# Kernel tuning notes

Hardware: AMD Instinct MI355X
Metric: run time of the kernel (lower is better)

Reference implementation:

```python
import jax, jax.numpy as jnp
import numpy as np

B, CIN, COUT = 8, 8, 8
NX, NT = 512, 512
M1, M2 = 4, 4


def setup_inputs() -> dict:
    key = jax.random.key(0)
    k1, k2, k3 = jax.random.split(key, 3)
    scale = 1.0 / (CIN * COUT)
    x = jax.random.normal(k1, (B, CIN, NX, NT), dtype=jnp.float32)
    T = jnp.arange(NT, dtype=jnp.float32).reshape(1, NT)  # time grid
    X = jnp.arange(NX, dtype=jnp.float32).reshape(1, NX)  # space grid
    weights1_ri = scale * jax.random.uniform(k2, (CIN, COUT, M1, M2, 2), dtype=jnp.float32)
    weights2_ri = scale * jax.random.uniform(k3, (CIN, COUT, M1, M2, 2), dtype=jnp.float32)
    return {"x": x, "T": T, "X": X, "weights1_ri": weights1_ri, "weights2_ri": weights2_ri}


def reference(x, T, X, weights1_ri, weights2_ri):
    # subsample every other grid point (as in the torch forward)
    xs = x[:, :, ::2, ::2]                      # [B, Cin, Hs, Ws]
    tx = T[:, ::2]                              # [1, Ws]
    ty = X[:, ::2]                              # [1, Hs]
    dty = ty[0, 1] - ty[0, 0]
    dtx = tx[0, 1] - tx[0, 0]
    Hs, Ws = xs.shape[-2], xs.shape[-1]
    Wr = Ws // 2 + 1

    FW1 = jnp.fft.rfft2(xs)                     # [B, Cin, Hs, Wr] complex64

    two_pi_i = 2.0 * jnp.pi * 1j
    lam1 = (jnp.fft.fftfreq(Hs).astype(jnp.float32) / dty).astype(jnp.complex64) * two_pi_i   # [Hs]
    lam2 = (jnp.fft.rfftfreq(Ws).astype(jnp.float32) / dtx).astype(jnp.complex64) * two_pi_i  # [Wr]

    w1 = (weights1_ri[..., 0] + 1j * weights1_ri[..., 1]).astype(jnp.complex64)
    w2 = (weights2_ri[..., 0] + 1j * weights2_ri[..., 1]).astype(jnp.complex64)

    out2 = jnp.zeros((xs.shape[0], w1.shape[1], Hs, Wr), dtype=jnp.complex64)
    out2 = out2.at[:, :, :M1, :M2].set(
        jnp.einsum('bixy,ioxy->boxy', FW1[:, :, :M1, :M2], w1))
    out2 = out2.at[:, :, -M1:, :M2].set(
        jnp.einsum('bixy,ioxy->boxy', FW1[:, :, -M1:, :M2], w2))

    # inverse transform onto the FULL (non-subsampled) grid via complex exponentials.
    # Same math as the original rank-4 term6 einsum, factorized separably.
    E1 = jnp.exp(lam1[:, None] * X.astype(jnp.complex64).reshape(1, -1))  # [Hs, NX]
    E2 = jnp.exp(lam2[:, None] * T.astype(jnp.complex64).reshape(1, -1))  # [Wr, NT]

    tmp = jnp.einsum('boxw,xz->bozw', out2, E1)   # [B, Cout, NX, Wr]
    x2 = jnp.einsum('bozw,wi->bozi', tmp, E2)     # [B, Cout, NX, NT]
    return jnp.real(x2) / (Ws * Hs)
```

## Files before the change

### kernel.cpp

```cpp
#include <hip/hip_runtime.h>
#include <hip/hip_bf16.h>


#define PI2 6.283185307179586f

__device__ __forceinline__ float foldred(float u, float v, int msk, int lane) {
    float send = (lane & msk) ? u : v;
    float recv = __shfl_xor(send, msk, 64);
    return ((lane & msk) ? v : u) + recv;
}

__global__ void k_dft_t(const float* __restrict__ x, float* __restrict__ pf) {
    int gid  = blockIdx.x * blockDim.x + threadIdx.x;
    int wid  = gid >> 6;
    int lane = gid & 63;
    int bc = wid >> 8;
    int y  = wid & 255;
    const float2* row2 = (const float2*)(x + ((size_t)bc * 512 + (size_t)(2 * y)) * 512);

    float v[4];
#pragma unroll
    for (int k = 0; k < 4; ++k) v[k] = row2[lane + 64 * k].x;

    float s, c;
    sincosf((PI2 / 256.0f) * (float)lane, &s, &c);
    float pr[4], pim[4];
    pr[0] = 1.f;                         pim[0] = 0.f;
    pr[1] = c;                           pim[1] = -s;
    pr[2] = pr[1]*pr[1] - pim[1]*pim[1]; pim[2] = 2.f*pr[1]*pim[1];
    pr[3] = pr[2]*pr[1] - pim[2]*pim[1]; pim[3] = pr[2]*pim[1] + pim[2]*pr[1];

    float ar[4] = {0.f,0.f,0.f,0.f};
    float ai[4] = {0.f,0.f,0.f,0.f};
#pragma unroll
    for (int k = 0; k < 4; ++k) {
#pragma unroll
        for (int kw = 0; kw < 4; ++kw) {
            int n = (k * kw) & 3;
            float rr, ri;
            if      (n == 0) { rr =  pr[kw];  ri =  pim[kw]; }
            else if (n == 1) { rr =  pim[kw]; ri = -pr[kw];  }
            else if (n == 2) { rr = -pr[kw];  ri = -pim[kw]; }
            else             { rr = -pim[kw]; ri =  pr[kw];  }
            ar[kw] += v[k] * rr;
            ai[kw] += v[k] * ri;
        }
    }
    float A0 = foldred(ar[0], ai[0], 1, lane);
    float A1 = foldred(ar[1], ai[1], 1, lane);
    float A2 = foldred(ar[2], ai[2], 1, lane);
    float A3 = foldred(ar[3], ai[3], 1, lane);
    float B0 = foldred(A0, A1, 2, lane);
    float B1 = foldred(A2, A3, 2, lane);
    float C  = foldred(B0, B1, 4, lane);
    C += __shfl_xor(C, 8, 64);
    C += __shfl_xor(C, 16, 64);
    C += __shfl_xor(C, 32, 64);
    if (lane < 8) {
        int kw = lane >> 1, ri = lane & 1;
        int b = bc >> 3, ci = bc & 7;
        pf[(((size_t)(b * 4 + kw) * 8 + ci) * 256 + y) * 2 + ri] = C;
    }
}

__global__ void k_mix_y(const float2* __restrict__ partial2, const float* __restrict__ w1,
                        const float* __restrict__ w2, float* __restrict__ c2f) {
    int gid  = blockIdx.x * blockDim.x + threadIdx.x;
    int wid  = gid >> 6;
    int lane = gid & 63;
    int o = wid & 7, midx = (wid >> 3) & 7, kw = (wid >> 6) & 3, b = wid >> 8;
    float m = (midx < 4) ? (float)midx : (float)(midx - 8);
    const float* w = (midx < 4) ? w1 : w2;
    int mx = midx & 3;

    float wr[8], wi[8];
#pragma unroll
    for (int ci = 0; ci < 8; ++ci) {
        const float* wp = w + ((((ci * 8 + o) * 4 + mx) * 4 + kw) * 2);
        wr[ci] = wp[0]; wi[ci] = wp[1];
    }

    float accx = 0.f, accy = 0.f;
#pragma unroll
    for (int k = 0; k < 4; ++k) {
        int y = lane + 64 * k;
        float sx = 0.f, sy = 0.f;
#pragma unroll
        for (int ci = 0; ci < 8; ++ci) {
            float2 p = partial2[((b * 4 + kw) * 8 + ci) * 256 + y];
            sx += p.x * wr[ci] - p.y * wi[ci];
            sy += p.x * wi[ci] + p.y * wr[ci];
        }
        float ang = (PI2 / 256.0f) * m * (float)y;
        float s, c;
        sincosf(ang, &s, &c);
        accx += sx * c + sy * s;
        accy += sy * c - sx * s;
    }
    float A = foldred(accx, accy, 1, lane);
    A += __shfl_xor(A, 2, 64);
    A += __shfl_xor(A, 4, 64);
    A += __shfl_xor(A, 8, 64);
    A += __shfl_xor(A, 16, 64);
    A += __shfl_xor(A, 32, 64);
    if (lane < 2)
        c2f[(((b * 8 + o) * 8 + midx) * 4 + kw) * 2 + lane] = A;
}

__global__ void k_eval2(const float2* __restrict__ c2, float* __restrict__ out) {
    int gid  = blockIdx.x * blockDim.x + threadIdx.x;
    int wid  = gid >> 6;
    int lane = gid & 63;
    int z  = wid & 255;
    int bo = wid >> 8;

    int ll = lane & 31;
    int kw = ll & 3, midx = (ll >> 2) & 7;
    float m = (midx < 4) ? (float)midx : (float)(midx - 8);
    float2 cc = c2[(bo * 8 + midx) * 4 + kw];
    float ang = (PI2 / 512.0f) * m * (float)z;
    float s, c;
    sincosf(ang, &s, &c);
    float hx = cc.x * c - cc.y * s;
    float hy = cc.x * s + cc.y * c;
    float sg = (midx & 1) ? -1.f : 1.f;
    float gx = sg * hx, gy = sg * hy;

    float F = foldred(hx, hy, 4, lane);
    F += __shfl_xor(F, 8, 64);
    F += __shfl_xor(F, 16, 64);
    float G = foldred(gx, gy, 4, lane);
    G += __shfl_xor(G, 8, 64);
    G += __shfl_xor(G, 16, 64);
    float h0x = __shfl(F, 0, 64);
    float h1x = __shfl(F, 1, 64), h2x = __shfl(F, 2, 64), h3x = __shfl(F, 3, 64);
    float h1y = __shfl(F, 5, 64), h2y = __shfl(F, 6, 64), h3y = __shfl(F, 7, 64);
    float g0x = __shfl(G, 0, 64);
    float g1x = __shfl(G, 1, 64), g2x = __shfl(G, 2, 64), g3x = __shfl(G, 3, 64);
    float g1y = __shfl(G, 5, 64), g2y = __shfl(G, 6, 64), g3y = __shfl(G, 7, 64);

    float* orow0 = out + (size_t)(bo * 512 + z) * 512;
    float* orow1 = orow0 + 256 * 512;
    const float inv = 1.0f / 65536.0f;

    float c1, s1;
    sincosf((PI2 / 512.0f) * (float)(lane * 4), &s1, &c1);
    const float cr = 0.99992470183839f;
    const float sr = 0.012271538285720f;

    float4 r0, r1, q0, q1;
    float* rp0 = &r0.x; float* rp1 = &r1.x;
    float* qp0 = &q0.x; float* qp1 = &q1.x;
#pragma unroll
    for (int j = 0; j < 4; ++j) {
        float c2a = c1 * c1 - s1 * s1, s2a = 2.f * c1 * s1;
        float c3a = c2a * c1 - s2a * s1, s3a = s2a * c1 + c2a * s1;
        float t1 = h1x * c1  - h1y * s1;
        float t2 = h2x * c2a - h2y * s2a;
        float t3 = h3x * c3a - h3y * s3a;
        rp0[j] = (h0x + t1 + t2 + t3) * inv;
        rp1[j] = (h0x - t1 + t2 - t3) * inv;
        float u1 = g1x * c1  - g1y * s1;
        float u2 = g2x * c2a - g2y * s2a;
        float u3 = g3x * c3a - g3y * s3a;
        qp0[j] = (g0x + u1 + u2 + u3) * inv;
        qp1[j] = (g0x - u1 + u2 - u3) * inv;
        float nc = c1 * cr - s1 * sr;
        float ns = s1 * cr + c1 * sr;
        c1 = nc; s1 = ns;
    }
    *(float4*)(orow0 + lane * 4)       = r0;
    *(float4*)(orow0 + 256 + lane * 4) = r1;
    *(float4*)(orow1 + lane * 4)       = q0;
    *(float4*)(orow1 + 256 + lane * 4) = q1;
}

extern "C" void kernel_launch(void* const* d_in, const int* in_sizes, int n_in,
                              void* d_out, int out_size, void* d_ws, size_t ws_size,
                              hipStream_t stream) {
    const float* x  = (const float*)d_in[0];
    const float* w1 = (const float*)d_in[3];
    const float* w2 = (const float*)d_in[4];
    float* out = (float*)d_out;

    float* partial2 = (float*)d_ws;
    float* c2f      = partial2 + 131072;

    k_dft_t<<<4096, 256, 0, stream>>>(x, partial2);
    k_mix_y<<<512, 256, 0, stream>>>((const float2*)partial2, w1, w2, c2f);
    k_eval2<<<4096, 256, 0, stream>>>((const float2*)c2f, out);
}
```

Baseline: 28.36 us.

## Fuse mode mixing and output evaluation into one kernel with redundant per-block mixing

```diff
diff --git a/kernel.cpp b/kernel.cpp
--- a/kernel.cpp
+++ b/kernel.cpp
@@ -63,116 +63,143 @@
     }
 }
 
-__global__ void k_mix_y(const float2* __restrict__ partial2, const float* __restrict__ w1,
-                        const float* __restrict__ w2, float* __restrict__ c2f) {
-    int gid  = blockIdx.x * blockDim.x + threadIdx.x;
-    int wid  = gid >> 6;
-    int lane = gid & 63;
-    int o = wid & 7, midx = (wid >> 3) & 7, kw = (wid >> 6) & 3, b = wid >> 8;
-    float m = (midx < 4) ? (float)midx : (float)(midx - 8);
-    const float* w = (midx < 4) ? w1 : w2;
-    int mx = midx & 3;
-
-    float wr[8], wi[8];
-#pragma unroll
-    for (int ci = 0; ci < 8; ++ci) {
-        const float* wp = w + ((((ci * 8 + o) * 4 + mx) * 4 + kw) * 2);
-        wr[ci] = wp[0]; wi[ci] = wp[1];
-    }
-
-    float accx = 0.f, accy = 0.f;
-#pragma unroll
-    for (int k = 0; k < 4; ++k) {
-        int y = lane + 64 * k;
-        float sx = 0.f, sy = 0.f;
-#pragma unroll
-        for (int ci = 0; ci < 8; ++ci) {
-            float2 p = partial2[((b * 4 + kw) * 8 + ci) * 256 + y];
-            sx += p.x * wr[ci] - p.y * wi[ci];
-            sy += p.x * wi[ci] + p.y * wr[ci];
-        }
-        float ang = (PI2 / 256.0f) * m * (float)y;
-        float s, c;
-        sincosf(ang, &s, &c);
-        accx += sx * c + sy * s;
-        accy += sy * c - sx * s;
-    }
-    float A = foldred(accx, accy, 1, lane);
-    A += __shfl_xor(A, 2, 64);
-    A += __shfl_xor(A, 4, 64);
-    A += __shfl_xor(A, 8, 64);
-    A += __shfl_xor(A, 16, 64);
-    A += __shfl_xor(A, 32, 64);
-    if (lane < 2)
-        c2f[(((b * 8 + o) * 8 + midx) * 4 + kw) * 2 + lane] = A;
-}
-
-__global__ void k_eval2(const float2* __restrict__ c2, float* __restrict__ out) {
-    int gid  = blockIdx.x * blockDim.x + threadIdx.x;
-    int wid  = gid >> 6;
-    int lane = gid & 63;
-    int z  = wid & 255;
-    int bo = wid >> 8;
+__global__ __launch_bounds__(256) void k_mix_eval(const float2* __restrict__ partial2,
+                                                  const float* __restrict__ w1,
+                                                  const float* __restrict__ w2,
+                                                  float* __restrict__ out) {
+    __shared__ float lcf[64];
+
+    int lane  = threadIdx.x & 63;
+    int w     = threadIdx.x >> 6;
+    int bo    = blockIdx.x >> 3;
+    int chunk = blockIdx.x & 7;
+    int b = bo >> 3, o = bo & 7;
+
+    {
+        float sb, cb;
+        sincosf((PI2 / 256.0f) * (float)lane, &sb, &cb);
+        float blr[5], bli[5];
+        blr[0] = 1.f; bli[0] = 0.f;
+        blr[1] = cb;  bli[1] = -sb;
+#pragma unroll
+        for (int q = 2; q <= 4; ++q) {
+            blr[q] = blr[q-1]*blr[1] - bli[q-1]*bli[1];
+            bli[q] = blr[q-1]*bli[1] + bli[q-1]*blr[1];
+        }
+
+#pragma unroll
+        for (int j = 0; j < 8; ++j) {
+            int idx  = w * 8 + j;
+            int midx = idx >> 2, kw = idx & 3;
+            int m  = (midx < 4) ? midx : midx - 8;
+            int am = (m < 0) ? -m : m;
+            float px = blr[am];
+            float py = (m < 0) ? -bli[am] : bli[am];
+            const float* wt = (midx < 4) ? w1 : w2;
+            int mx = midx & 3;
+
+            float wr[8], wi[8];
+#pragma unroll
+            for (int ci = 0; ci < 8; ++ci) {
+                const float* wp = wt + ((((ci * 8 + o) * 4 + mx) * 4 + kw) * 2);
+                wr[ci] = wp[0]; wi[ci] = wp[1];
+            }
+
+            float accx = 0.f, accy = 0.f;
+#pragma unroll
+            for (int k = 0; k < 4; ++k) {
+                int y = lane + 64 * k;
+                float sx = 0.f, sy = 0.f;
+#pragma unroll
+                for (int ci = 0; ci < 8; ++ci) {
+                    float2 p = partial2[((b * 4 + kw) * 8 + ci) * 256 + y];
+                    sx += p.x * wr[ci] - p.y * wi[ci];
+                    sy += p.x * wi[ci] + p.y * wr[ci];
+                }
+                int n = (m * k) & 3;
+                float tx = px, ty = py;
+                if (n & 1) { float t = tx; tx = ty; ty = -t; }
+                if (n & 2) { tx = -tx; ty = -ty; }
+                accx += sx * tx - sy * ty;
+                accy += sx * ty + sy * tx;
+            }
+            float A = foldred(accx, accy, 1, lane);
+            A += __shfl_xor(A, 2, 64);
+            A += __shfl_xor(A, 4, 64);
+            A += __shfl_xor(A, 8, 64);
+            A += __shfl_xor(A, 16, 64);
+            A += __shfl_xor(A, 32, 64);
+            if (lane < 2) lcf[idx * 2 + lane] = A;
+        }
+    }
+    __syncthreads();
+
+    float c1b, s1b;
+    sincosf((PI2 / 512.0f) * (float)(lane * 4), &s1b, &c1b);
+    const float cr = 0.99992470183839f;
+    const float sr = 0.012271538285720f;
+    const float inv = 1.0f / 65536.0f;
 
     int ll = lane & 31;
     int kw = ll & 3, midx = (ll >> 2) & 7;
     float m = (midx < 4) ? (float)midx : (float)(midx - 8);
-    float2 cc = c2[(bo * 8 + midx) * 4 + kw];
-    float ang = (PI2 / 512.0f) * m * (float)z;
-    float s, c;
-    sincosf(ang, &s, &c);
-    float hx = cc.x * c - cc.y * s;
-    float hy = cc.x * s + cc.y * c;
-    float sg = (midx & 1) ? -1.f : 1.f;
-    float gx = sg * hx, gy = sg * hy;
-
-    float F = foldred(hx, hy, 4, lane);
-    F += __shfl_xor(F, 8, 64);
-    F += __shfl_xor(F, 16, 64);
-    float G = foldred(gx, gy, 4, lane);
-    G += __shfl_xor(G, 8, 64);
-    G += __shfl_xor(G, 16, 64);
-    float h0x = __shfl(F, 0, 64);
-    float h1x = __shfl(F, 1, 64), h2x = __shfl(F, 2, 64), h3x = __shfl(F, 3, 64);
-    float h1y = __shfl(F, 5, 64), h2y = __shfl(F, 6, 64), h3y = __shfl(F, 7, 64);
-    float g0x = __shfl(G, 0, 64);
-    float g1x = __shfl(G, 1, 64), g2x = __shfl(G, 2, 64), g3x = __shfl(G, 3, 64);
-    float g1y = __shfl(G, 5, 64), g2y = __shfl(G, 6, 64), g3y = __shfl(G, 7, 64);
-
-    float* orow0 = out + (size_t)(bo * 512 + z) * 512;
-    float* orow1 = orow0 + 256 * 512;
-    const float inv = 1.0f / 65536.0f;
-
-    float c1, s1;
-    sincosf((PI2 / 512.0f) * (float)(lane * 4), &s1, &c1);
-    const float cr = 0.99992470183839f;
-    const float sr = 0.012271538285720f;
-
-    float4 r0, r1, q0, q1;
-    float* rp0 = &r0.x; float* rp1 = &r1.x;
-    float* qp0 = &q0.x; float* qp1 = &q1.x;
-#pragma unroll
-    for (int j = 0; j < 4; ++j) {
-        float c2a = c1 * c1 - s1 * s1, s2a = 2.f * c1 * s1;
-        float c3a = c2a * c1 - s2a * s1, s3a = s2a * c1 + c2a * s1;
-        float t1 = h1x * c1  - h1y * s1;
-        float t2 = h2x * c2a - h2y * s2a;
-        float t3 = h3x * c3a - h3y * s3a;
-        rp0[j] = (h0x + t1 + t2 + t3) * inv;
-        rp1[j] = (h0x - t1 + t2 - t3) * inv;
-        float u1 = g1x * c1  - g1y * s1;
-        float u2 = g2x * c2a - g2y * s2a;
-        float u3 = g3x * c3a - g3y * s3a;
-        qp0[j] = (g0x + u1 + u2 + u3) * inv;
-        qp1[j] = (g0x - u1 + u2 - u3) * inv;
-        float nc = c1 * cr - s1 * sr;
-        float ns = s1 * cr + c1 * sr;
-        c1 = nc; s1 = ns;
-    }
-    *(float4*)(orow0 + lane * 4)       = r0;
-    *(float4*)(orow0 + 256 + lane * 4) = r1;
-    *(float4*)(orow1 + lane * 4)       = q0;
-    *(float4*)(orow1 + 256 + lane * 4) = q1;
+    float2 cc = make_float2(lcf[ll * 2], lcf[ll * 2 + 1]);
+    float sgm = (midx & 1) ? -1.f : 1.f;
+
+#pragma unroll
+    for (int e = 0; e < 8; ++e) {
+        int z = chunk * 32 + w * 8 + e;
+
+        float ang = (PI2 / 512.0f) * m * (float)z;
+        float s, c;
+        sincosf(ang, &s, &c);
+        float hx = cc.x * c - cc.y * s;
+        float hy = cc.x * s + cc.y * c;
+        float gx = sgm * hx, gy = sgm * hy;
+
+        float F = foldred(hx, hy, 4, lane);
+        F += __shfl_xor(F, 8, 64);
+        F += __shfl_xor(F, 16, 64);
+        float G = foldred(gx, gy, 4, lane);
+        G += __shfl_xor(G, 8, 64);
+        G += __shfl_xor(G, 16, 64);
+        float h0x = __shfl(F, 0, 64);
+        float h1x = __shfl(F, 1, 64), h2x = __shfl(F, 2, 64), h3x = __shfl(F, 3, 64);
+        float h1y = __shfl(F, 5, 64), h2y = __shfl(F, 6, 64), h3y = __shfl(F, 7, 64);
+        float g0x = __shfl(G, 0, 64);
+        float g1x = __shfl(G, 1, 64), g2x = __shfl(G, 2, 64), g3x = __shfl(G, 3, 64);
+        float g1y = __shfl(G, 5, 64), g2y = __shfl(G, 6, 64), g3y = __shfl(G, 7, 64);
+
+        float* orow0 = out + (size_t)(bo * 512 + z) * 512;
+        float* orow1 = orow0 + 256 * 512;
+
+        float c1 = c1b, s1 = s1b;
+        float4 r0, r1, q0, q1;
+        float* rp0 = &r0.x; float* rp1 = &r1.x;
+        float* qp0 = &q0.x; float* qp1 = &q1.x;
+#pragma unroll
+        for (int j = 0; j < 4; ++j) {
+            float c2a = c1 * c1 - s1 * s1, s2a = 2.f * c1 * s1;
+            float c3a = c2a * c1 - s2a * s1, s3a = s2a * c1 + c2a * s1;
+            float t1 = h1x * c1  - h1y * s1;
+            float t2 = h2x * c2a - h2y * s2a;
+            float t3 = h3x * c3a - h3y * s3a;
+            rp0[j] = (h0x + t1 + t2 + t3) * inv;
+            rp1[j] = (h0x - t1 + t2 - t3) * inv;
+            float u1 = g1x * c1  - g1y * s1;
+            float u2 = g2x * c2a - g2y * s2a;
+            float u3 = g3x * c3a - g3y * s3a;
+            qp0[j] = (g0x + u1 + u2 + u3) * inv;
+            qp1[j] = (g0x - u1 + u2 - u3) * inv;
+            float nc = c1 * cr - s1 * sr;
+            float ns = s1 * cr + c1 * sr;
+            c1 = nc; s1 = ns;
+        }
+        *(float4*)(orow0 + lane * 4)       = r0;
+        *(float4*)(orow0 + 256 + lane * 4) = r1;
+        *(float4*)(orow1 + lane * 4)       = q0;
+        *(float4*)(orow1 + 256 + lane * 4) = q1;
+    }
 }
 
 extern "C" void kernel_launch(void* const* d_in, const int* in_sizes, int n_in,
@@ -183,10 +210,8 @@
     const float* w2 = (const float*)d_in[4];
     float* out = (float*)d_out;
 
-    float* partial2 = (float*)d_ws;
-    float* c2f      = partial2 + 131072;
-
-    k_dft_t<<<4096, 256, 0, stream>>>(x, partial2);
-    k_mix_y<<<512, 256, 0, stream>>>((const float2*)partial2, w1, w2, c2f);
-    k_eval2<<<4096, 256, 0, stream>>>((const float2*)c2f, out);
-}
+    float* pf = (float*)d_ws;
+
+    k_dft_t<<<4096, 256, 0, stream>>>(x, pf);
+    k_mix_eval<<<512, 256, 0, stream>>>((const float2*)pf, w1, w2, out);
+}
```

Result: slower. 41.06 us (+44.8%).
